# Kernel optimization log

Measured on AMD Instinct MI355X. Metric: run time of the kernel, lower is better.

The kernel has to match this reference:

```python
import jax, jax.numpy as jnp
import numpy as np

B, L, D, H = 4, 1024, 256, 8
TEMP = float(np.sqrt(D))
EPS_SM = 1e-6
EPS_LN = 1e-5


def setup_inputs() -> dict:
    key = jax.random.key(0)
    ks = jax.random.split(key, 8)
    std = float(np.sqrt(2.0 / (D * 2)))
    return {
        "q": jax.random.normal(ks[0], (B, L, D), jnp.float32),
        "mask": jax.random.randint(ks[1], (B, L, L), 0, 2, jnp.int32),
        "k": jax.random.normal(ks[2], (B, L, D), jnp.float32),
        "v": jax.random.normal(ks[3], (B, L, D), jnp.float32),
        "w_qs": jax.random.normal(ks[4], (H * D, D), jnp.float32) * std,
        "w_ks": jax.random.normal(ks[5], (H * D, D), jnp.float32) * std,
        "w_vs": jax.random.normal(ks[6], (H * D, D), jnp.float32) * std,
        "fc_w": jax.random.normal(ks[7], (D, H * D), jnp.float32) * float(np.sqrt(2.0 / (D + H * D))),
        "fc_b": jnp.zeros((D,), jnp.float32),
        "ln_g": jnp.ones((D,), jnp.float32),
        "ln_b": jnp.zeros((D,), jnp.float32),
    }


def masked_softmax(x, m):
    # repo's layers.masked_softmax: clamp, mask-mul, stable exp, mask-mul, normalize
    x = jnp.clip(x, -15.0, 15.0) * m
    e = jnp.exp(x - jnp.max(x, axis=-1, keepdims=True)) * m
    return e / (jnp.sum(e, axis=-1, keepdims=True) + EPS_SM)


def reference(q, mask, k, v, w_qs, w_ks, w_vs, fc_w, fc_b, ln_g, ln_b):
    residual = q
    m = mask.astype(q.dtype)[:, None, :, :]          # [B,1,Lq,Lk]
    # projections to per-head full-dim: [B,L,H,D]
    qh = (q @ w_qs.T).reshape(B, L, H, D)
    kh = (k @ w_ks.T).reshape(B, L, H, D)
    vh = (v @ w_vs.T).reshape(B, L, H, D)
    scores = jnp.einsum("bqhd,bkhd->bhqk", qh, kh) / TEMP   # [B,H,Lq,Lk]
    attn = masked_softmax(scores, m)
    out = jnp.einsum("bhqk,bkhd->bqhd", attn, vh).reshape(B, L, H * D)
    out = out @ fc_w.T + fc_b                         # [B,L,D]
    out = out + residual
    mu = jnp.mean(out, axis=-1, keepdims=True)
    var = jnp.var(out, axis=-1, keepdims=True)
    out = (out - mu) / jnp.sqrt(var + EPS_LN) * ln_g + ln_b
    # match torch attn layout: [H*B, Lq, Lk] (head-major)
    attn_hb = jnp.transpose(attn, (1, 0, 2, 3)).reshape(H * B, L, L)
    return out, attn_hb
```

## Files before the change

### kernel.cpp

```cpp
#include <hip/hip_runtime.h>
#include <cstdint>
#include <math.h>

#define Bsz 4
#define Lsz 1024
#define Dsz 256
#define Hsz 8
#define HD  2048
#define NROWS (Bsz*Lsz)
#define INV_TEMP 0.0625f

typedef __attribute__((ext_vector_type(8))) short bf16x8;
typedef __attribute__((ext_vector_type(4))) float f32x4;

__device__ inline unsigned short f2bf(float f) {
    union { float f; unsigned u; } x; x.f = f;
    unsigned r = x.u + 0x7fffu + ((x.u >> 16) & 1u);
    return (unsigned short)(r >> 16);
}
__device__ inline float bf2f(unsigned short u) {
    union { unsigned u; float f; } x; x.u = (unsigned)u << 16; return x.f;
}

#define GBL(p) ((const __attribute__((address_space(1))) unsigned int*)(p))
#define LDS(p) ((__attribute__((address_space(3))) unsigned int*)(p))

template<int N> __device__ __forceinline__ void vmw() {
    if constexpr (N == 0)       asm volatile("s_waitcnt vmcnt(0)"  ::: "memory");
    else if constexpr (N == 4)  asm volatile("s_waitcnt vmcnt(4)"  ::: "memory");
    else if constexpr (N == 6)  asm volatile("s_waitcnt vmcnt(6)"  ::: "memory");
    else if constexpr (N == 10) asm volatile("s_waitcnt vmcnt(10)" ::: "memory");
    else if constexpr (N == 14) asm volatile("s_waitcnt vmcnt(14)" ::: "memory");
    else static_assert(N == 0, "unsupported vmcnt literal");
}

template <int TMv, int TNv, typename OutT, int EPI, int MINW, bool FUSE>
__global__ __launch_bounds__(256, MINW) void gemm_bt(
    const unsigned short* __restrict__ A, const unsigned short* __restrict__ Bm,
    OutT* __restrict__ C,
    int K, int lda, int ldb, int ldc, int inner,
    long long sA1, long long sA2, long long sB1, long long sB2,
    long long sC1, long long sC2, float alpha,
    const unsigned short* __restrict__ maskb, long long sM2,
    const float* __restrict__ invs, long long sI1, long long sI2,
    float* __restrict__ aux,
    const unsigned short* __restrict__ A2, const unsigned short* __restrict__ B2,
    unsigned short* __restrict__ C2)
{
    constexpr int WMv = TMv / 2, WNv = TNv / 2;
    constexpr int IT = TMv / 32, JT = TNv / 32;
    constexpr int APASS = TMv / 32, NPASS = (TMv + TNv) / 32;
    constexpr int TILE = (TMv + TNv) * 64;
    static_assert(NPASS == 6 || NPASS == 10, "vmcnt literals assume NPASS in {6,10}");

    const int z  = blockIdx.z;
    int mx = blockIdx.x, my = blockIdx.y;

    if constexpr (FUSE) {
        if (z >= 2) {
            const int idx = my * 64 + mx;
            if (idx >= 256) return;
            mx = idx & 31; my = idx >> 5;
            const int b = z - 2;
            A   = A2;
            Bm  = B2 + (size_t)b * ((size_t)Lsz * Dsz);
            C   = (OutT*)(C2 + (size_t)b * ((size_t)HD * Lsz));
            ldc = Lsz;
        } else {
            A  += (size_t)z * sA2;
            Bm += (size_t)z * sB2;
            C  += (size_t)z * sC2;
        }
    } else {
        const int i1 = z / inner;
        const int i2 = z % inner;
        A  += (size_t)i1 * sA1 + (size_t)i2 * sA2;
        Bm += (size_t)i1 * sB1 + (size_t)i2 * sB2;
        C  += (size_t)i1 * sC1 + (size_t)i2 * sC2;
        if (EPI == 1) { maskb += (size_t)i2 * sM2; aux += (size_t)z * Lsz; }
        if (EPI == 2) { invs  += (size_t)i1 * sI1 + (size_t)i2 * sI2; aux += (size_t)z * Lsz * Lsz; }
    }

    __shared__ unsigned short S[2 * TILE];

    const int t    = threadIdx.x;
    const int lane = t & 63;
    const int w    = t >> 6;
    const int wm   = w & 1;
    const int wn   = w >> 1;
    const int m0   = mx * TMv;
    const int n0   = my * TNv;

    const int rA = t >> 3;
    const int ch = ((t & 7) ^ (rA & 7)) * 8;
    const unsigned short* gA = A  + (size_t)(m0 + rA) * lda + ch;
    const unsigned short* gB = Bm + (size_t)(n0 + rA) * ldb + ch;

    const int fr = lane & 15;
    const int q  = lane >> 4;

    f32x4 acc[IT][JT];
#pragma unroll
    for (int i = 0; i < IT; ++i)
#pragma unroll
        for (int j = 0; j < JT; ++j) acc[i][j] = (f32x4){0.f, 0.f, 0.f, 0.f};

    auto stage = [&](unsigned short* Sb, int k0) {
#pragma unroll
        for (int p = 0; p < NPASS; ++p) {
            const unsigned short* src = (p < APASS)
                ? (gA + (size_t)p * 32 * lda + k0)
                : (gB + (size_t)(p - APASS) * 32 * ldb + k0);
            __builtin_amdgcn_global_load_lds(GBL(src), LDS(Sb + p * 2048 + t * 8), 16, 0, 0);
        }
    };
    auto kstep = [&](const unsigned short* As) {
        const unsigned short* Bs = As + TMv * 64;
#pragma unroll
        for (int ks = 0; ks < 2; ++ks) {
            const int slot = ((ks * 4 + q) ^ (fr & 7)) * 8;
            bf16x8 a[IT], b[JT];
#pragma unroll
            for (int i = 0; i < IT; ++i)
                a[i] = *(const bf16x8*)(As + (wm * WMv + i * 16 + fr) * 64 + slot);
#pragma unroll
            for (int j = 0; j < JT; ++j)
                b[j] = *(const bf16x8*)(Bs + (wn * WNv + j * 16 + fr) * 64 + slot);
#pragma unroll
            for (int i = 0; i < IT; ++i)
#pragma unroll
                for (int j = 0; j < JT; ++j)
                    acc[i][j] = __builtin_amdgcn_mfma_f32_16x16x32_bf16(a[i], b[j], acc[i][j], 0, 0, 0);
        }
    };

    const int nk = K >> 6;

    float ainv[EPI == 2 ? (TMv / 32) : 1];
    if constexpr (EPI == 2) {
        const int rsub = lane >> 3;
#pragma unroll
        for (int pass = 0; pass < TMv / 32; ++pass)
            ainv[pass] = 1.0f / (invs[m0 + w * (TMv / 4) + pass * 8 + rsub] + 1e-6f);
    }

    stage(S, 0);

    for (int kt = 0; kt < nk; ++kt) {
        if (kt + 1 < nk) stage(S + ((kt + 1) & 1) * TILE, (kt + 1) << 6);

        if constexpr (EPI == 2) {
            if (kt + 1 < nk) { if (kt >= 1) vmw<NPASS + 4>(); else vmw<NPASS>(); }
            else             { if (kt >= 1) vmw<4>();         else vmw<0>(); }
        } else {
            if (kt + 1 < nk) vmw<NPASS>(); else vmw<0>();
        }
        __builtin_amdgcn_s_barrier();

        kstep(S + (kt & 1) * TILE);

        if constexpr (EPI == 2) {
            const unsigned short* As = S + (kt & 1) * TILE;
            const int chunk = lane & 7;
            const int rsub  = lane >> 3;
#pragma unroll
            for (int pass = 0; pass < TMv / 32; ++pass) {
                const int row = w * (TMv / 4) + pass * 8 + rsub;
                const uint4 u = *(const uint4*)(As + row * 64 + ((chunk ^ (row & 7)) * 8));
                const float iv = ainv[pass];
                float4 lo, hi;
                lo.x = bf2f((unsigned short)(u.x & 0xffff)) * iv; lo.y = bf2f((unsigned short)(u.x >> 16)) * iv;
                lo.z = bf2f((unsigned short)(u.y & 0xffff)) * iv; lo.w = bf2f((unsigned short)(u.y >> 16)) * iv;
                hi.x = bf2f((unsigned short)(u.z & 0xffff)) * iv; hi.y = bf2f((unsigned short)(u.z >> 16)) * iv;
                hi.z = bf2f((unsigned short)(u.w & 0xffff)) * iv; hi.w = bf2f((unsigned short)(u.w >> 16)) * iv;
                float* op = aux + (size_t)(m0 + row) * Lsz + (kt << 6) + chunk * 8;
                *(float4*)op = lo;
                *(float4*)(op + 4) = hi;
            }
        }

        asm volatile("s_waitcnt lgkmcnt(0)" ::: "memory");
        __builtin_amdgcn_s_barrier();
    }

    float einv[EPI == 2 ? IT : 1][EPI == 2 ? 4 : 1];
    if constexpr (EPI == 2) {
#pragma unroll
        for (int i = 0; i < IT; ++i)
#pragma unroll
            for (int r = 0; r < 4; ++r)
                einv[i][r] = 1.0f / (invs[m0 + wm * WMv + i * 16 + q * 4 + r] + 1e-6f);
    }

#pragma unroll
    for (int i = 0; i < IT; ++i) {
#pragma unroll
        for (int r = 0; r < 4; ++r) {
            const int row = m0 + wm * WMv + i * 16 + q * 4 + r;
            float rsum = 0.f;
#pragma unroll
            for (int j = 0; j < JT; ++j) {
                const int col = n0 + wn * WNv + j * 16 + fr;
                float vv = acc[i][j][r] * alpha;
                if (EPI == 0) {
                    if constexpr (sizeof(OutT) == 4)
                        C[(size_t)row * ldc + col] = (OutT)vv;
                    else
                        ((unsigned short*)C)[(size_t)row * ldc + col] = f2bf(vv);
                } else if (EPI == 1) {
                    const float m = bf2f(maskb[(size_t)row * Lsz + col]);
                    vv = fminf(fmaxf(vv, -15.f), 15.f) * m;
                    vv = __expf(vv) * m;
                    const unsigned short us = f2bf(vv);
                    ((unsigned short*)C)[(size_t)row * ldc + col] = us;
                    rsum += bf2f(us);
                } else {
                    vv *= einv[i][r];
                    ((unsigned short*)C)[(size_t)row * ldc + col] = f2bf(vv);
                }
            }
            if constexpr (EPI == 1) {
#pragma unroll
                for (int o = 1; o <= 8; o <<= 1) rsum += __shfl_xor(rsum, o, 64);
                if (fr == 0) atomicAdd(&aux[row], rsum);
            }
        }
    }
}

__global__ __launch_bounds__(256) void cast_all(
    const float* __restrict__ q, const float* __restrict__ k, const float* __restrict__ v,
    const float* __restrict__ wq, const float* __restrict__ wk, const float* __restrict__ wv,
    const float* __restrict__ fw, const int* __restrict__ mask,
    unsigned short* __restrict__ qb, unsigned short* __restrict__ kb, unsigned short* __restrict__ vb,
    unsigned short* __restrict__ wqb, unsigned short* __restrict__ wkb, unsigned short* __restrict__ wvb,
    unsigned short* __restrict__ fwb, unsigned short* __restrict__ mb,
    float* __restrict__ rs)
{
    const int gid = blockIdx.x * 256 + threadIdx.x;
    const int NQ = 262144;
    const int NW = 131072;
    const int NF = 3 * NQ + 4 * NW;
    const int NM = 1048576;
    if (gid >= NF) {
        const int off = gid - NF;
        if (off >= NM) {
            const int ri = off - NM;
            if (ri < 8192) ((float4*)rs)[ri] = (float4){0.f, 0.f, 0.f, 0.f};
            return;
        }
        const int4 mi = ((const int4*)mask)[off];
        ushort4 o;
        o.x = mi.x ? 0x3F80 : 0;
        o.y = mi.y ? 0x3F80 : 0;
        o.z = mi.z ? 0x3F80 : 0;
        o.w = mi.w ? 0x3F80 : 0;
        ((ushort4*)mb)[off] = o;
        return;
    }
    const float* src; unsigned short* dst; int off;
    if      (gid < NQ)            { src = q;  dst = qb;  off = gid; }
    else if (gid < 2 * NQ)        { src = k;  dst = kb;  off = gid - NQ; }
    else if (gid < 3 * NQ)        { src = v;  dst = vb;  off = gid - 2 * NQ; }
    else if (gid < 3 * NQ + NW)   { src = wq; dst = wqb; off = gid - 3 * NQ; }
    else if (gid < 3 * NQ + 2*NW) { src = wk; dst = wkb; off = gid - 3 * NQ - NW; }
    else if (gid < 3 * NQ + 3*NW) { src = wv; dst = wvb; off = gid - 3 * NQ - 2 * NW; }
    else                          { src = fw; dst = fwb; off = gid - 3 * NQ - 3 * NW; }
    float4 f = ((const float4*)src)[off];
    ushort4 o;
    o.x = f2bf(f.x); o.y = f2bf(f.y); o.z = f2bf(f.z); o.w = f2bf(f.w);
    ((ushort4*)dst)[off] = o;
}

__global__ __launch_bounds__(256) void ln_kernel(const float* __restrict__ gout,
                                                 const float* __restrict__ qin,
                                                 const float* __restrict__ fc_b,
                                                 const float* __restrict__ ln_g,
                                                 const float* __restrict__ ln_b,
                                                 float* __restrict__ out)
{
    const int row = blockIdx.x;
    const int t = threadIdx.x;
    const size_t idx = (size_t)row * Dsz + t;
    const size_t P = (size_t)NROWS * Dsz;
    const float val = gout[idx] + gout[idx + P] + gout[idx + 2 * P] + gout[idx + 3 * P]
                    + fc_b[t] + qin[idx];

    __shared__ float red[4];
    float s = val;
#pragma unroll
    for (int o = 32; o > 0; o >>= 1) s += __shfl_down(s, o, 64);
    const int lane = t & 63, w = t >> 6;
    if (lane == 0) red[w] = s;
    __syncthreads();
    const float mu = (red[0] + red[1] + red[2] + red[3]) * (1.0f / Dsz);
    __syncthreads();

    float d = val - mu;
    float s2 = d * d;
#pragma unroll
    for (int o = 32; o > 0; o >>= 1) s2 += __shfl_down(s2, o, 64);
    if (lane == 0) red[w] = s2;
    __syncthreads();
    const float var = (red[0] + red[1] + red[2] + red[3]) * (1.0f / Dsz);

    out[idx] = d * rsqrtf(var + 1e-5f) * ln_g[t] + ln_b[t];
}

extern "C" void kernel_launch(void* const* d_in, const int* in_sizes, int n_in,
                              void* d_out, int out_size, void* d_ws, size_t ws_size,
                              hipStream_t stream)
{
    const float* q    = (const float*)d_in[0];
    const int*   mask = (const int*)d_in[1];
    const float* k    = (const float*)d_in[2];
    const float* v    = (const float*)d_in[3];
    const float* w_qs = (const float*)d_in[4];
    const float* w_ks = (const float*)d_in[5];
    const float* w_vs = (const float*)d_in[6];
    const float* fc_w = (const float*)d_in[7];
    const float* fc_b = (const float*)d_in[8];
    const float* ln_g = (const float*)d_in[9];
    const float* ln_b = (const float*)d_in[10];

    float* out  = (float*)d_out;
    float* attn = (float*)d_out + (size_t)NROWS * Dsz;

    unsigned short* wsu = (unsigned short*)d_ws;
    unsigned short* qh     = wsu;
    unsigned short* kh     = qh + (size_t)NROWS * HD;
    unsigned short* q_bf   = kh + (size_t)NROWS * HD;
    unsigned short* k_bf   = q_bf + (size_t)NROWS * Dsz;
    unsigned short* v_bf   = k_bf + (size_t)NROWS * Dsz;
    unsigned short* wq_bf  = v_bf + (size_t)NROWS * Dsz;
    unsigned short* wk_bf  = wq_bf + (size_t)HD * Dsz;
    unsigned short* wv_bf  = wk_bf + (size_t)HD * Dsz;
    unsigned short* vt     = wv_bf + (size_t)HD * Dsz;
    unsigned short* attn_e = vt + (size_t)Bsz * HD * Lsz;
    unsigned short* attnv  = attn_e + (size_t)32 * Lsz * Lsz;
    unsigned short* fcw_bf = attnv + (size_t)NROWS * HD;
    float*          rowsum = (float*)(fcw_bf + (size_t)Dsz * HD);
    float*          fcout  = rowsum + 32768;
    unsigned short* maskb  = (unsigned short*)(fcout + (size_t)4 * NROWS * Dsz);

    dim3 blk(256);

    cast_all<<<dim3(9248), blk, 0, stream>>>(q, k, v, w_qs, w_ks, w_vs, fc_w, mask,
                                             q_bf, k_bf, v_bf, wq_bf, wk_bf, wv_bf, fcw_bf, maskb,
                                             rowsum);

    {
        dim3 grid(NROWS / 64, HD / 128, 6);
        gemm_bt<64, 128, unsigned short, 0, 3, true><<<grid, blk, 0, stream>>>(q_bf, wq_bf, qh,
            Dsz, Dsz, Dsz, HD, 2,
            0, (long long)NROWS * Dsz, 0, (long long)HD * Dsz, 0, (long long)NROWS * HD,
            1.0f, nullptr, 0, nullptr, 0, 0, nullptr,
            wv_bf, v_bf, vt);
    }

    {
        dim3 grid(Lsz / 64, Lsz / 128, Hsz * Bsz);
        gemm_bt<64, 128, unsigned short, 1, 3, false><<<grid, blk, 0, stream>>>(qh, kh, attn_e,
            Dsz, HD, HD, Lsz, Bsz,
            Dsz, (long long)Lsz * HD, Dsz, (long long)Lsz * HD,
            (long long)Bsz * Lsz * Lsz, (long long)Lsz * Lsz,
            INV_TEMP, maskb, (long long)Lsz * Lsz, nullptr, 0, 0, rowsum,
            nullptr, nullptr, nullptr);
    }

    {
        dim3 grid(Lsz / 64, 1, Hsz * Bsz);
        gemm_bt<64, 256, unsigned short, 2, 2, false><<<grid, blk, 0, stream>>>(attn_e, vt, attnv,
            Lsz, Lsz, Lsz, HD, Bsz,
            (long long)Bsz * Lsz * Lsz, (long long)Lsz * Lsz,
            (long long)Dsz * Lsz, (long long)HD * Lsz,
            Dsz, (long long)Lsz * HD,
            1.0f, nullptr, 0, rowsum, (long long)Bsz * Lsz, (long long)Lsz, attn,
            nullptr, nullptr, nullptr);
    }

    {
        dim3 grid(NROWS / 64, Dsz / 128, 4);
        gemm_bt<64, 128, float, 0, 3, false><<<grid, blk, 0, stream>>>(attnv, fcw_bf, fcout,
            512, HD, HD, Dsz, 4,
            0, 512, 0, 512, 0, (long long)NROWS * Dsz,
            1.0f, nullptr, 0, nullptr, 0, 0, nullptr,
            nullptr, nullptr, nullptr);
    }

    ln_kernel<<<dim3(NROWS), blk, 0, stream>>>(fcout, q, fc_b, ln_g, ln_b, out);
}
```

Measured before the change: 331.2 us.

## Add XCD-aware block swizzle and shrink mask to uint8

Remaps the linear block id so that consecutive tiles sharing operands land on the same XCD, aiming to improve L2 reuse across MI355X's chiplets in all four GEMM launches. It also stores the converted mask as one byte per element instead of a bf16, halving the mask write in the cast kernel and the mask read in the scores epilogue. An explicit vmcnt(0) wait is added after the reciprocal row-sum loads in the attn@V kernel, which appears to guard the hand-counted vmcnt waits in the k-loop. The swizzle relies on grid dimensions passed as template parameters matching the launch grids.

New measurement: 328.0 us. Within noise of the previous version (-1.0%).

```diff
diff --git a/kernel.cpp b/kernel.cpp
--- a/kernel.cpp
+++ b/kernel.cpp
@@ -34,14 +34,15 @@
     else static_assert(N == 0, "unsupported vmcnt literal");
 }
 
-template <int TMv, int TNv, typename OutT, int EPI, int MINW, bool FUSE>
+template <int TMv, int TNv, typename OutT, int EPI, int MINW, bool FUSE,
+          int GX, int GY, int GZ>
 __global__ __launch_bounds__(256, MINW) void gemm_bt(
     const unsigned short* __restrict__ A, const unsigned short* __restrict__ Bm,
     OutT* __restrict__ C,
     int K, int lda, int ldb, int ldc, int inner,
     long long sA1, long long sA2, long long sB1, long long sB2,
     long long sC1, long long sC2, float alpha,
-    const unsigned short* __restrict__ maskb, long long sM2,
+    const unsigned char* __restrict__ maskb, long long sM2,
     const float* __restrict__ invs, long long sI1, long long sI2,
     float* __restrict__ aux,
     const unsigned short* __restrict__ A2, const unsigned short* __restrict__ B2,
@@ -51,10 +52,16 @@
     constexpr int IT = TMv / 32, JT = TNv / 32;
     constexpr int APASS = TMv / 32, NPASS = (TMv + TNv) / 32;
     constexpr int TILE = (TMv + TNv) * 64;
+    constexpr int G = GX * GY * GZ;
+    static_assert(G % 8 == 0, "bijective XCD swizzle needs G%8==0");
     static_assert(NPASS == 6 || NPASS == 10, "vmcnt literals assume NPASS in {6,10}");
 
-    const int z  = blockIdx.z;
-    int mx = blockIdx.x, my = blockIdx.y;
+    const int lid = blockIdx.x + GX * (blockIdx.y + GY * blockIdx.z);
+    const int nid = (lid & 7) * (G >> 3) + (lid >> 3);
+    int mx = nid % GX;
+    const int t1g = nid / GX;
+    int my = t1g % GY;
+    const int z  = t1g / GY;
 
     if constexpr (FUSE) {
         if (z >= 2) {
@@ -142,6 +149,7 @@
 #pragma unroll
         for (int pass = 0; pass < TMv / 32; ++pass)
             ainv[pass] = 1.0f / (invs[m0 + w * (TMv / 4) + pass * 8 + rsub] + 1e-6f);
+        vmw<0>();
     }
 
     stage(S, 0);
@@ -208,7 +216,7 @@
                     else
                         ((unsigned short*)C)[(size_t)row * ldc + col] = f2bf(vv);
                 } else if (EPI == 1) {
-                    const float m = bf2f(maskb[(size_t)row * Lsz + col]);
+                    const float m = (float)maskb[(size_t)row * Lsz + col];
                     vv = fminf(fmaxf(vv, -15.f), 15.f) * m;
                     vv = __expf(vv) * m;
                     const unsigned short us = f2bf(vv);
@@ -234,7 +242,7 @@
     const float* __restrict__ fw, const int* __restrict__ mask,
     unsigned short* __restrict__ qb, unsigned short* __restrict__ kb, unsigned short* __restrict__ vb,
     unsigned short* __restrict__ wqb, unsigned short* __restrict__ wkb, unsigned short* __restrict__ wvb,
-    unsigned short* __restrict__ fwb, unsigned short* __restrict__ mb,
+    unsigned short* __restrict__ fwb, unsigned char* __restrict__ mb,
     float* __restrict__ rs)
 {
     const int gid = blockIdx.x * 256 + threadIdx.x;
@@ -250,12 +258,12 @@
             return;
         }
         const int4 mi = ((const int4*)mask)[off];
-        ushort4 o;
-        o.x = mi.x ? 0x3F80 : 0;
-        o.y = mi.y ? 0x3F80 : 0;
-        o.z = mi.z ? 0x3F80 : 0;
-        o.w = mi.w ? 0x3F80 : 0;
-        ((ushort4*)mb)[off] = o;
+        uchar4 o;
+        o.x = mi.x ? 1 : 0;
+        o.y = mi.y ? 1 : 0;
+        o.z = mi.z ? 1 : 0;
+        o.w = mi.w ? 1 : 0;
+        ((uchar4*)mb)[off] = o;
         return;
     }
     const float* src; unsigned short* dst; int off;
@@ -341,7 +349,7 @@
     unsigned short* fcw_bf = attnv + (size_t)NROWS * HD;
     float*          rowsum = (float*)(fcw_bf + (size_t)Dsz * HD);
     float*          fcout  = rowsum + 32768;
-    unsigned short* maskb  = (unsigned short*)(fcout + (size_t)4 * NROWS * Dsz);
+    unsigned char*  maskb  = (unsigned char*)(fcout + (size_t)4 * NROWS * Dsz);
 
     dim3 blk(256);
 
@@ -351,7 +359,8 @@
 
     {
         dim3 grid(NROWS / 64, HD / 128, 6);
-        gemm_bt<64, 128, unsigned short, 0, 3, true><<<grid, blk, 0, stream>>>(q_bf, wq_bf, qh,
+        gemm_bt<64, 128, unsigned short, 0, 3, true, 64, 16, 6><<<grid, blk, 0, stream>>>(
+            q_bf, wq_bf, qh,
             Dsz, Dsz, Dsz, HD, 2,
             0, (long long)NROWS * Dsz, 0, (long long)HD * Dsz, 0, (long long)NROWS * HD,
             1.0f, nullptr, 0, nullptr, 0, 0, nullptr,
@@ -360,7 +369,8 @@
 
     {
         dim3 grid(Lsz / 64, Lsz / 128, Hsz * Bsz);
-        gemm_bt<64, 128, unsigned short, 1, 3, false><<<grid, blk, 0, stream>>>(qh, kh, attn_e,
+        gemm_bt<64, 128, unsigned short, 1, 3, false, 16, 8, 32><<<grid, blk, 0, stream>>>(
+            qh, kh, attn_e,
             Dsz, HD, HD, Lsz, Bsz,
             Dsz, (long long)Lsz * HD, Dsz, (long long)Lsz * HD,
             (long long)Bsz * Lsz * Lsz, (long long)Lsz * Lsz,
@@ -370,7 +380,8 @@
 
     {
         dim3 grid(Lsz / 64, 1, Hsz * Bsz);
-        gemm_bt<64, 256, unsigned short, 2, 2, false><<<grid, blk, 0, stream>>>(attn_e, vt, attnv,
+        gemm_bt<64, 256, unsigned short, 2, 2, false, 16, 1, 32><<<grid, blk, 0, stream>>>(
+            attn_e, vt, attnv,
             Lsz, Lsz, Lsz, HD, Bsz,
             (long long)Bsz * Lsz * Lsz, (long long)Lsz * Lsz,
             (long long)Dsz * Lsz, (long long)HD * Lsz,
@@ -381,7 +392,8 @@
 
     {
         dim3 grid(NROWS / 64, Dsz / 128, 4);
-        gemm_bt<64, 128, float, 0, 3, false><<<grid, blk, 0, stream>>>(attnv, fcw_bf, fcout,
+        gemm_bt<64, 128, float, 0, 3, false, 64, 2, 4><<<grid, blk, 0, stream>>>(
+            attnv, fcw_bf, fcout,
             512, HD, HD, Dsz, 4,
             0, 512, 0, 512, 0, (long long)NROWS * Dsz,
             1.0f, nullptr, 0, nullptr, 0, 0, nullptr,
```
